# Kernel optimization log

Hardware: AMD Instinct MI355X
Metric: run time of the kernel (lower is better)

The kernel has to match this reference:

```python
import jax, jax.numpy as jnp
import numpy as np

PRE_NMS_TOPN = 12000
POST_NMS_TOPN = 2000
NMS_THRESH = 0.7
IM_SIZE = 1024
BATCH = 16
FPN_SCALES = np.array([8.0, 16.0, 32.0, 64.0, 128.0])
FPN_STRIDES = np.array([4, 8, 16, 32, 64])
RATIOS = np.array([0.5, 1.0, 2.0])
FEAT_SHAPES = [(IM_SIZE // s, IM_SIZE // s) for s in FPN_STRIDES]


def _anchors_single(scale, ratios, shape, stride):
    # faithful to generate_anchors_single_pyramid (mask-rcnn/FPN style)
    heights = scale / np.sqrt(ratios)
    widths = scale * np.sqrt(ratios)
    shifts_y = np.arange(0, shape[0]) * stride
    shifts_x = np.arange(0, shape[1]) * stride
    sx, sy = np.meshgrid(shifts_x, shifts_y)
    bw, bcx = np.meshgrid(widths, sx.flatten())
    bh, bcy = np.meshgrid(heights, sy.flatten())
    centers = np.stack([bcy, bcx], axis=2).reshape(-1, 2)
    sizes = np.stack([bh, bw], axis=2).reshape(-1, 2)
    return np.concatenate([centers - 0.5 * sizes, centers + 0.5 * sizes], axis=1)


def generate_anchors_all_pyramids():
    levels = [_anchors_single(FPN_SCALES[i], RATIOS, FEAT_SHAPES[i], FPN_STRIDES[i]) for i in range(5)]
    return np.concatenate(levels, axis=0).astype(np.float32)  # [261888, 4]


def setup_inputs() -> dict:
    key = jax.random.key(0)
    k1, k2 = jax.random.split(key)
    anchors = jnp.asarray(generate_anchors_all_pyramids())
    n = anchors.shape[0]
    scores = jax.random.uniform(k1, (BATCH, n), dtype=jnp.float32)
    bbox_deltas = jax.random.normal(k2, (BATCH, n, 4), dtype=jnp.float32) * 0.1
    im_info = jnp.tile(jnp.array([[IM_SIZE, IM_SIZE, 1.0]], dtype=jnp.float32), (BATCH, 1))
    return {"scores": scores, "bbox_deltas": bbox_deltas, "im_info": im_info, "anchors": anchors}


def _bbox_transform_inv(anchors, deltas):
    # anchors [N,4], deltas [B,N,4] -> [B,N,4]
    w = anchors[:, 2] - anchors[:, 0] + 1.0
    h = anchors[:, 3] - anchors[:, 1] + 1.0
    cx = anchors[:, 0] + 0.5 * w
    cy = anchors[:, 1] + 0.5 * h
    dx, dy, dw, dh = deltas[..., 0], deltas[..., 1], deltas[..., 2], deltas[..., 3]
    pcx = dx * w + cx
    pcy = dy * h + cy
    pw = jnp.exp(dw) * w
    ph = jnp.exp(dh) * h
    return jnp.stack([pcx - 0.5 * pw, pcy - 0.5 * ph, pcx + 0.5 * pw, pcy + 0.5 * ph], axis=-1)


def _clip_boxes(boxes, im_info):
    xmax = (im_info[:, 1] - 1.0)[:, None]
    ymax = (im_info[:, 0] - 1.0)[:, None]
    x1 = jnp.clip(boxes[..., 0], 0.0, xmax)
    y1 = jnp.clip(boxes[..., 1], 0.0, ymax)
    x2 = jnp.clip(boxes[..., 2], 0.0, xmax)
    y2 = jnp.clip(boxes[..., 3], 0.0, ymax)
    return jnp.stack([x1, y1, x2, y2], axis=-1)


def _nms_single(boxes):
    # boxes [P,4] sorted by score desc; greedy IoU suppression, keep POST_NMS_TOPN
    x1, y1, x2, y2 = boxes[:, 0], boxes[:, 1], boxes[:, 2], boxes[:, 3]
    areas = (x2 - x1 + 1.0) * (y2 - y1 + 1.0)

    def step(valid, _):
        any_valid = jnp.any(valid)
        idx = jnp.argmax(valid)  # first surviving box (sorted order)
        xx1 = jnp.maximum(x1[idx], x1)
        yy1 = jnp.maximum(y1[idx], y1)
        xx2 = jnp.minimum(x2[idx], x2)
        yy2 = jnp.minimum(y2[idx], y2)
        inter = jnp.maximum(xx2 - xx1 + 1.0, 0.0) * jnp.maximum(yy2 - yy1 + 1.0, 0.0)
        iou = inter / (areas[idx] + areas - inter)
        valid = valid & (iou <= NMS_THRESH)  # suppresses idx itself (IoU=1)
        return valid, jnp.where(any_valid, idx, -1)

    valid0 = jnp.ones(boxes.shape[0], dtype=bool)
    _, keep = jax.lax.scan(step, valid0, None, length=POST_NMS_TOPN)
    return keep  # [POST_NMS_TOPN] int, -1 = padding


def reference(scores, bbox_deltas, im_info, anchors):
    b = scores.shape[0]
    proposals = _bbox_transform_inv(anchors, bbox_deltas)  # [B,N,4]
    proposals = _clip_boxes(proposals, im_info)
    _, order = jax.lax.top_k(scores, PRE_NMS_TOPN)  # descending sort + pre-NMS cut
    props = jnp.take_along_axis(proposals, order[..., None], axis=1)  # [B,P,4]
    keep = jax.vmap(_nms_single)(props)  # [B,POST_NMS_TOPN]
    mask = (keep >= 0)
    kept = jnp.take_along_axis(props, jnp.maximum(keep, 0)[..., None], axis=1)
    kept = kept * mask[..., None].astype(props.dtype)  # zero-pad like output.zero_()
    batch_col = jnp.broadcast_to(jnp.arange(b, dtype=props.dtype)[:, None, None], (b, POST_NMS_TOPN, 1))
    return jnp.concatenate([batch_col, kept], axis=-1)  # [B,2000,5]
```

## Files before the change

kernel.cpp:

```cpp
#include <hip/hip_runtime.h>
#include <stdint.h>
#include <math.h>

#define NANCH 261888
#define NBATCH 16
#define PRE_NMS 12000
#define POST_NMS 2000
#define NBINS 21845
#define BINCAP 98304
#define NCHUNK 188
#define VBINS 4096
#define CANDCAP 16384
#define ADJR 12
#define OVFCAP 4096

__device__ __forceinline__ uint64_t make_key(float s, int i) {
    uint32_t u = __float_as_uint(s);
    u ^= (u >> 31) ? 0xFFFFFFFFu : 0x80000000u;
    return ((uint64_t)u << 32) | (uint32_t)(~(uint32_t)i);
}

__device__ __forceinline__ bool kill_pair(float4 a, float4 c) {
    const double MD = (double)0.7f + 2.9802322387695312e-08;
    float xx1 = fmaxf(a.x, c.x), yy1 = fmaxf(a.y, c.y);
    float xx2 = fminf(a.z, c.z), yy2 = fminf(a.w, c.w);
    float ww = fmaxf(__fadd_rn(__fsub_rn(xx2, xx1), 1.0f), 0.0f);
    float hh = fmaxf(__fadd_rn(__fsub_rn(yy2, yy1), 1.0f), 0.0f);
    float inter = __fmul_rn(ww, hh);
    float aa = __fmul_rn(__fadd_rn(__fsub_rn(a.z, a.x), 1.0f),
                         __fadd_rn(__fsub_rn(a.w, a.y), 1.0f));
    float ab = __fmul_rn(__fadd_rn(__fsub_rn(c.z, c.x), 1.0f),
                         __fadd_rn(__fsub_rn(c.w, c.y), 1.0f));
    float denom = __fsub_rn(__fadd_rn(aa, ab), inter);
    return !((double)inter < MD * (double)denom);
}

__device__ __forceinline__ int vbucket(float s) {
    int bk = (int)(s * 4096.0f);
    return min(max(bk, 0), VBINS - 1);
}

__global__ void k_init(uint32_t* hist, uint32_t* cnt, uint32_t* ccnt,
                       uint32_t* ovfc, uint32_t* deg) {
    int tid = blockIdx.x * 256 + threadIdx.x;
    int stride = gridDim.x * 256;
    for (int i = tid; i < NBATCH * VBINS; i += stride) hist[i] = 0;
    for (int i = tid; i < NBATCH * PRE_NMS; i += stride) deg[i] = 0;
    if (tid < NBATCH) { cnt[tid] = 0; ccnt[tid] = 0; ovfc[tid] = 0; }
}

__global__ __launch_bounds__(256) void k_histv(const float* __restrict__ scores,
                                               uint32_t* __restrict__ hist) {
    __shared__ uint32_t lh[VBINS];
    int tid = threadIdx.x;
    int b = blockIdx.y;
    for (int i = tid; i < VBINS; i += 256) lh[i] = 0;
    __syncthreads();
    const float* sc = scores + (size_t)b * NANCH;
    for (int i = blockIdx.x * 256 + tid; i < NANCH; i += gridDim.x * 256)
        atomicAdd(&lh[vbucket(sc[i])], 1u);
    __syncthreads();
    for (int i = tid; i < VBINS; i += 256) {
        uint32_t c = lh[i];
        if (c) atomicAdd(&hist[b * VBINS + i], c);
    }
}

__global__ __launch_bounds__(64) void k_pickv(const uint32_t* __restrict__ hist,
                                              uint32_t* __restrict__ Bsel) {
    int b = blockIdx.x;
    int ln = threadIdx.x;
    const uint32_t* h = hist + b * VBINS;
    int hi = VBINS - 1 - 64 * ln;
    uint32_t tot = 0;
    for (int k = 0; k < 64; ++k) tot += h[hi - k];
    uint32_t x = tot;
    for (int d = 1; d < 64; d <<= 1) { uint32_t y = __shfl_up(x, d); if (ln >= d) x += y; }
    uint32_t excl = x - tot;
    bool hitc = (excl < (uint32_t)PRE_NMS) && (excl + tot >= (uint32_t)PRE_NMS);
    unsigned long long bal = __ballot(hitc);
    int L = __ffsll(bal) - 1;
    if (ln == L) {
        uint32_t cum = excl;
        for (int k = 0; k < 64; ++k) {
            int bin = hi - k;
            uint32_t c = h[bin];
            if (cum + c >= (uint32_t)PRE_NMS) { Bsel[b] = (uint32_t)bin; break; }
            cum += c;
        }
    }
}

__global__ __launch_bounds__(256) void k_splitv(const float* __restrict__ scores,
                                                const uint32_t* __restrict__ Bsel,
                                                uint32_t* __restrict__ cnt,
                                                uint32_t* __restrict__ ccnt,
                                                uint64_t* __restrict__ selk,
                                                uint64_t* __restrict__ candbuf) {
    __shared__ uint64_t lbuf[2048];
    __shared__ uint32_t lcnt, lccnt, lbase, lcbase;
    int tid = threadIdx.x;
    int b = blockIdx.y;
    int ln = tid & 63;
    if (tid == 0) { lcnt = 0; lccnt = 0; }
    __syncthreads();
    uint32_t B = Bsel[b];
    const float* sc = scores + (size_t)b * NANCH;
    int base0 = blockIdx.x * 2048;
    for (int r = 0; r < 8; ++r) {
        int i = base0 + r * 256 + tid;
        bool psel = false, pcand = false;
        uint64_t key = 0;
        if (i < NANCH) {
            float s = sc[i];
            int bk = vbucket(s);
            psel = ((uint32_t)bk > B);
            pcand = ((uint32_t)bk == B);
            if (psel || pcand) key = make_key(s, i);
        }
        unsigned long long bs = __ballot(psel);
        uint32_t wb = 0;
        if (ln == 0 && bs) wb = atomicAdd(&lcnt, (uint32_t)__popcll(bs));
        wb = __shfl(wb, 0);
        if (psel) lbuf[wb + (uint32_t)__popcll(bs & ((1ull << ln) - 1ull))] = key;
        unsigned long long bcm = __ballot(pcand);
        uint32_t wc = 0;
        if (ln == 0 && bcm) wc = atomicAdd(&lccnt, (uint32_t)__popcll(bcm));
        wc = __shfl(wc, 0);
        if (pcand) lbuf[2047 - (wc + (uint32_t)__popcll(bcm & ((1ull << ln) - 1ull)))] = key;
    }
    __syncthreads();
    if (tid == 0) {
        lbase = lcnt ? atomicAdd(&cnt[b], lcnt) : 0u;
        lcbase = lccnt ? atomicAdd(&ccnt[b], lccnt) : 0u;
    }
    __syncthreads();
    uint32_t n = lcnt, bsx = lbase;
    for (uint32_t i = tid; i < n; i += 256)
        selk[(size_t)b * PRE_NMS + bsx + i] = lbuf[i];
    uint32_t nc = lccnt, bcx = lcbase;
    for (uint32_t i = tid; i < nc; i += 256) {
        uint32_t p = bcx + i;
        if (p < CANDCAP) candbuf[(size_t)b * CANDCAP + p] = lbuf[2047 - i];
    }
}

__global__ __launch_bounds__(1024) void k_rankb(const uint64_t* __restrict__ selk,
                                                const uint64_t* __restrict__ candbuf,
                                                const uint32_t* __restrict__ cnt,
                                                const uint32_t* __restrict__ ccnt,
                                                uint32_t* __restrict__ aidx) {
    __shared__ uint64_t kys[PRE_NMS];
    __shared__ uint32_t bbase[2048];
    __shared__ uint32_t bcur[2048];
    __shared__ uint16_t blist[PRE_NMS];
    __shared__ float redf[32];
    __shared__ uint32_t wsum[16];
    __shared__ uint32_t appcnt;
    int b = blockIdx.x, t = threadIdx.x, wv = t >> 6, ln = t & 63;
    const uint64_t* sk = selk + (size_t)b * PRE_NMS;
    const uint64_t* cb = candbuf + (size_t)b * CANDCAP;
    int nc = (int)cnt[b];
    int m = (int)min(ccnt[b], (uint32_t)CANDCAP);
    uint32_t nd = (uint32_t)(PRE_NMS - nc);
    if (t == 0) appcnt = 0;
    for (int i = t; i < 2048; i += 1024) bcur[i] = 0;
    float lmin = 1e30f, lmax = -1e30f;
    for (int i = t; i < nc; i += 1024) {
        uint64_t k = sk[i];
        kys[i] = k;
        float s = __uint_as_float((uint32_t)(k >> 32) ^ 0x80000000u);
        lmin = fminf(lmin, s); lmax = fmaxf(lmax, s);
    }
    __syncthreads();
    for (int i = t; i < m; i += 1024) {
        uint64_t ki = cb[i];
        int rk = 0;
        for (int j = 0; j < m; ++j) rk += (cb[j] > ki) ? 1 : 0;
        if ((uint32_t)rk < nd) {
            uint32_t pos = (uint32_t)nc + atomicAdd(&appcnt, 1u);
            kys[pos] = ki;
            float s = __uint_as_float((uint32_t)(ki >> 32) ^ 0x80000000u);
            lmin = fminf(lmin, s); lmax = fmaxf(lmax, s);
        }
    }
    for (int d = 1; d < 64; d <<= 1) {
        lmin = fminf(lmin, __shfl_xor(lmin, d));
        lmax = fmaxf(lmax, __shfl_xor(lmax, d));
    }
    if (ln == 0) { redf[wv] = lmin; redf[16 + wv] = lmax; }
    __syncthreads();
    float smin = redf[0], smax = redf[16];
    for (int w = 1; w < 16; ++w) { smin = fminf(smin, redf[w]); smax = fmaxf(smax, redf[16 + w]); }
    float scale = 2047.0f / fmaxf(smax - smin, 1e-20f);
    for (int i = t; i < PRE_NMS; i += 1024) {
        float s = __uint_as_float((uint32_t)(kys[i] >> 32) ^ 0x80000000u);
        int bk = min(max((int)((s - smin) * scale), 0), 2047);
        atomicAdd(&bcur[bk], 1u);
    }
    __syncthreads();
    {
        int r0 = 2 * t;
        uint32_t a0 = bcur[2047 - r0];
        uint32_t a1 = bcur[2046 - r0];
        uint32_t tot = a0 + a1;
        uint32_t x = tot;
        for (int d = 1; d < 64; d <<= 1) { uint32_t y = __shfl_up(x, d); if (ln >= d) x += y; }
        if (ln == 63) wsum[wv] = x;
        __syncthreads();
        uint32_t wb = 0;
        for (int w = 0; w < 16; ++w) wb += (w < wv) ? wsum[w] : 0u;
        uint32_t excl = wb + x - tot;
        bbase[2047 - r0] = excl;
        bbase[2046 - r0] = excl + a0;
        bcur[2047 - r0] = excl;
        bcur[2046 - r0] = excl + a0;
    }
    __syncthreads();
    for (int i = t; i < PRE_NMS; i += 1024) {
        float s = __uint_as_float((uint32_t)(kys[i] >> 32) ^ 0x80000000u);
        int bk = min(max((int)((s - smin) * scale), 0), 2047);
        uint32_t pos = atomicAdd(&bcur[bk], 1u);
        blist[pos] = (uint16_t)i;
    }
    __syncthreads();
    for (int i = t; i < PRE_NMS; i += 1024) {
        uint64_t ki = kys[i];
        float s = __uint_as_float((uint32_t)(ki >> 32) ^ 0x80000000u);
        int bk = min(max((int)((s - smin) * scale), 0), 2047);
        uint32_t start = bbase[bk], end = bcur[bk];
        int rk = 0;
        for (uint32_t p = start; p < end; ++p) {
            int j = (int)blist[p];
            rk += (kys[j] > ki) ? 1 : 0;
        }
        aidx[(size_t)b * PRE_NMS + bbase[bk] + (uint32_t)rk] = ~(uint32_t)(ki & 0xFFFFFFFFull);
    }
}

__global__ void k_gather(const float4* __restrict__ anchors, const float4* __restrict__ deltas,
                         const float* __restrict__ im_info, const uint32_t* __restrict__ aidx,
                         float4* __restrict__ props) {
    int b = blockIdx.y;
    int i = blockIdx.x * 256 + threadIdx.x;
    if (i >= PRE_NMS) return;
    uint32_t a = aidx[(size_t)b * PRE_NMS + i];
    float4 an = anchors[a];
    float4 dl = deltas[(size_t)b * NANCH + a];
    float w  = __fadd_rn(__fsub_rn(an.z, an.x), 1.0f);
    float h  = __fadd_rn(__fsub_rn(an.w, an.y), 1.0f);
    float cx = __fadd_rn(an.x, __fmul_rn(0.5f, w));
    float cy = __fadd_rn(an.y, __fmul_rn(0.5f, h));
    float pcx = __fadd_rn(__fmul_rn(dl.x, w), cx);
    float pcy = __fadd_rn(__fmul_rn(dl.y, h), cy);
    float ew = (float)exp((double)dl.z);
    float eh = (float)exp((double)dl.w);
    float pw = __fmul_rn(ew, w);
    float ph = __fmul_rn(eh, h);
    float x1 = __fsub_rn(pcx, __fmul_rn(0.5f, pw));
    float y1 = __fsub_rn(pcy, __fmul_rn(0.5f, ph));
    float x2 = __fadd_rn(pcx, __fmul_rn(0.5f, pw));
    float y2 = __fadd_rn(pcy, __fmul_rn(0.5f, ph));
    float xmax = __fsub_rn(im_info[b * 3 + 1], 1.0f);
    float ymax = __fsub_rn(im_info[b * 3 + 0], 1.0f);
    x1 = fminf(fmaxf(x1, 0.0f), xmax);
    y1 = fminf(fmaxf(y1, 0.0f), ymax);
    x2 = fminf(fmaxf(x2, 0.0f), xmax);
    y2 = fminf(fmaxf(y2, 0.0f), ymax);
    props[(size_t)b * PRE_NMS + i] = make_float4(x1, y1, x2, y2);
}

__device__ __forceinline__ int bucket_of(float w) {
    int iw = (int)w;
    int bb = 31 - __clz(iw);
    return min(max(bb, 2), 9);
}
__device__ __forceinline__ int grid_base(int g) {
    return (65536 - (65536 >> ((g - 2) * 2))) / 3;
}

__global__ __launch_bounds__(1024) void k_binfused(const float4* __restrict__ props,
                                                   uint32_t* __restrict__ binoff,
                                                   uint16_t* __restrict__ binlist) {
    __shared__ uint32_t bc[NBINS];
    __shared__ uint32_t wsum[16];
    int b = blockIdx.x, t = threadIdx.x, wv = t >> 6, ln = t & 63;
    for (int i = t; i < NBINS; i += 1024) bc[i] = 0;
    __syncthreads();
    const float4* pb = props + (size_t)b * PRE_NMS;
    for (int i = t; i < PRE_NMS; i += 1024) {
        float4 p = pb[i];
        float w = __fadd_rn(__fsub_rn(p.z, p.x), 1.0f);
        int bb = bucket_of(w);
        int cs = bb + 1, dim = 128 >> (bb - 2);
        int gb = grid_base(bb);
        int cx0 = ((int)p.x) >> cs, cx1 = ((int)p.z) >> cs;
        int cy0 = ((int)p.y) >> cs, cy1 = ((int)p.w) >> cs;
        for (int cy = cy0; cy <= cy1; ++cy)
            for (int cx = cx0; cx <= cx1; ++cx)
                atomicAdd(&bc[gb + cy * dim + cx], 1u);
    }
    __syncthreads();
    {
        const int PER = 22;
        int i0 = t * PER;
        uint32_t v[PER];
        uint32_t tot = 0;
        #pragma unroll
        for (int k = 0; k < PER; ++k) { int i = i0 + k; v[k] = (i < NBINS) ? bc[i] : 0; tot += v[k]; }
        uint32_t x = tot;
        for (int d = 1; d < 64; d <<= 1) { uint32_t y = __shfl_up(x, d); if (ln >= d) x += y; }
        if (ln == 63) wsum[wv] = x;
        __syncthreads();
        uint32_t wb = 0;
        for (int w = 0; w < 16; ++w) wb += (w < wv) ? wsum[w] : 0u;
        uint32_t run = wb + x - tot;
        uint32_t* offb = binoff + (size_t)b * (NBINS + 1);
        #pragma unroll
        for (int k = 0; k < PER; ++k) {
            int i = i0 + k;
            if (i < NBINS) { offb[i] = run; bc[i] = run; run += v[k]; }
        }
        if (t == 1023) offb[NBINS] = run;
    }
    __syncthreads();
    uint16_t* bl = binlist + (size_t)b * BINCAP;
    for (int i = t; i < PRE_NMS; i += 1024) {
        float4 p = pb[i];
        float w = __fadd_rn(__fsub_rn(p.z, p.x), 1.0f);
        int bb = bucket_of(w);
        int cs = bb + 1, dim = 128 >> (bb - 2);
        int gb = grid_base(bb);
        int cx0 = ((int)p.x) >> cs, cx1 = ((int)p.z) >> cs;
        int cy0 = ((int)p.y) >> cs, cy1 = ((int)p.w) >> cs;
        for (int cy = cy0; cy <= cy1; ++cy)
            for (int cx = cx0; cx <= cx1; ++cx) {
                uint32_t pos = atomicAdd(&bc[gb + cy * dim + cx], 1u);
                uint32_t e = (uint32_t)i | ((cx == cx0) ? 0x4000u : 0u)
                                        | ((cy == cy0) ? 0x8000u : 0u);
                if (pos < BINCAP) bl[pos] = (uint16_t)e;
            }
    }
}

__global__ __launch_bounds__(256) void k_search(const float4* __restrict__ props,
                                                const uint32_t* __restrict__ binoff,
                                                const uint16_t* __restrict__ binlist,
                                                uint32_t* __restrict__ deg,
                                                uint16_t* __restrict__ adjfix,
                                                uint32_t* __restrict__ ovf,
                                                uint32_t* __restrict__ ovfcnt) {
    int L = blockIdx.x;
    int b = L & (NBATCH - 1);
    int t = threadIdx.x;
    int i = (L >> 4) * 128 + (t >> 1);
    int half = t & 1;
    if (i >= PRE_NMS) return;
    const float4* pb = props + (size_t)b * PRE_NMS;
    float4 pi = pb[i];
    float wi = __fadd_rn(__fsub_rn(pi.z, pi.x), 1.0f);
    float hi = __fadd_rn(__fsub_rn(pi.w, pi.y), 1.0f);
    int bb = bucket_of(wi);
    const uint32_t* ob = binoff + (size_t)b * (NBINS + 1);
    const uint16_t* bl = binlist + (size_t)b * BINCAP;
    uint32_t* degb = deg + (size_t)b * PRE_NMS;
    uint16_t* adjb = adjfix + (size_t)b * PRE_NMS * ADJR;
    uint32_t* ovfb = ovf + (size_t)b * OVFCAP;
    float ex0 = fmaxf(__fsub_rn(pi.x, 1.0f), 0.0f);
    float ey0 = fmaxf(__fsub_rn(pi.y, 1.0f), 0.0f);
    float ex1 = fminf(__fadd_rn(pi.z, 1.0f), 1023.0f);
    float ey1 = fminf(__fadd_rn(pi.w, 1.0f), 1023.0f);

    auto add_edge = [&](int r, int n) {
        uint32_t s = atomicAdd(&degb[r], 1u);
        if (s < ADJR) {
            adjb[(size_t)r * ADJR + s] = (uint16_t)n;
        } else {
            uint32_t p = atomicAdd(&ovfcnt[b], 1u);
            if (p < OVFCAP) ovfb[p] = ((uint32_t)r << 16) | (uint32_t)n;
        }
    };

    #pragma unroll
    for (int pass = 0; pass < 2; ++pass) {
        int g = (pass == 0) ? bb : bb - 1;
        bool tie = (pass == 0);
        if (g < 2) continue;
        int cs = g + 1, dim = 128 >> (g - 2);
        int gb2 = grid_base(g);
        int sx0 = ((int)ex0) >> cs, sx1 = ((int)ex1) >> cs;
        int sy0 = ((int)ey0) >> cs, sy1 = ((int)ey1) >> cs;
        for (int cy = sy0; cy <= sy1; ++cy)
            for (int cx = sx0; cx <= sx1; ++cx) {
                int bin = gb2 + cy * dim + cx;
                uint32_t k0 = ob[bin], k1 = ob[bin + 1];
                for (uint32_t k = k0 + (uint32_t)half; k < k1; k += 2) {
                    uint32_t ent = bl[k];
                    int j = (int)(ent & 0x3FFFu);
                    if (tie && j <= i) continue;
                    if (!((cx == sx0) || (ent & 0x4000u))) continue;
                    if (!((cy == sy0) || (ent & 0x8000u))) continue;
                    float4 pj = pb[j];
                    float wj = __fadd_rn(__fsub_rn(pj.z, pj.x), 1.0f);
                    float hj = __fadd_rn(__fsub_rn(pj.w, pj.y), 1.0f);
                    if (fminf(wi, wj) < 0.6f * fmaxf(wi, wj)) continue;
                    if (fminf(hi, hj) < 0.6f * fmaxf(hi, hj)) continue;
                    if (kill_pair(pi, pj)) {
                        add_edge(i, j);
                        add_edge(j, i);
                    }
                }
            }
    }
}

__global__ __launch_bounds__(64) void k_greedy(const uint32_t* __restrict__ deg,
                                               const uint16_t* __restrict__ adjfix,
                                               const uint32_t* __restrict__ ovf,
                                               const uint32_t* __restrict__ ovfcnt,
                                               const float4* __restrict__ props,
                                               float* __restrict__ out) {
    int b = blockIdx.x;
    int ln = threadIdx.x;
    __shared__ uint32_t mask[375];
    __shared__ int keeps[POST_NMS];
    for (int i = ln; i < 375; i += 64) mask[i] = 0xFFFFFFFFu;
    const uint32_t* degb = deg + (size_t)b * PRE_NMS;
    const uint32_t* roww = (const uint32_t*)(adjfix + (size_t)b * PRE_NMS * ADJR);
    const uint32_t* ovfb = ovf + (size_t)b * OVFCAP;
    int novf = (int)min(ovfcnt[b], (uint32_t)OVFCAP);
    int nsel = 0;
    uint32_t dcur = (ln < PRE_NMS) ? degb[ln] : 0u;
    uint32_t w[6];
    #pragma unroll
    for (int k = 0; k < 6; ++k) w[k] = (ln < PRE_NMS) ? roww[(size_t)ln * 6 + k] : 0u;
    for (int c = 0; c < NCHUNK && nsel < POST_NMS; ++c) {
        int rn = (c + 1) * 64 + ln;
        uint32_t dnxt = 0, wn[6] = {0, 0, 0, 0, 0, 0};
        if (rn < PRE_NMS) {
            dnxt = degb[rn];
            #pragma unroll
            for (int k = 0; k < 6; ++k) wn[k] = roww[(size_t)rn * 6 + k];
        }
        int r = c * 64 + ln;
        bool inb = (r < PRE_NMS);
        int nfix = inb ? min((int)dcur, ADJR) : 0;
        uint32_t base = (uint32_t)(c * 64);
        uint64_t K = 0;
        #pragma unroll
        for (int k = 0; k < ADJR; ++k) {
            if (k < nfix) {
                uint32_t e = (w[k >> 1] >> ((k & 1) * 16)) & 0xFFFFu;
                uint32_t d = e - base;
                if (d < 64u) K |= (1ull << d);
            }
        }
        if (novf && inb) {
            for (int k = 0; k < novf; ++k) {
                uint32_t e = ovfb[k];
                if ((int)(e >> 16) == r) {
                    uint32_t d = (e & 0xFFFFu) - base;
                    if (d < 64u) K |= (1ull << d);
                }
            }
        }
        int vbit = inb ? (int)((mask[r >> 5] >> (r & 31)) & 1u) : 0;
        uint64_t valid = (uint64_t)__ballot(vbit);
        uint32_t Klo = (uint32_t)K, Khi = (uint32_t)(K >> 32);
        uint64_t todo = valid & (uint64_t)__ballot(K != 0);
        while (todo) {
            int s = __ffsll((unsigned long long)todo) - 1;
            if ((valid >> s) & 1ull) {
                uint32_t kl = (uint32_t)__builtin_amdgcn_readlane((int)Klo, s);
                uint32_t kh = (uint32_t)__builtin_amdgcn_readlane((int)Khi, s);
                valid &= ~(((uint64_t)kh << 32) | (uint64_t)kl);
            }
            todo &= (todo - 1);
            todo &= valid;
        }
        uint64_t acc = valid;
        int cnt2 = __popcll(acc);
        int myacc = (int)((acc >> ln) & 1ull);
        uint64_t ltm = (ln == 0) ? 0ull : (~0ull >> (64 - ln));
        int pos = nsel + __popcll(acc & ltm);
        bool eff = myacc && (pos < POST_NMS);
        if (eff) {
            keeps[pos] = r;
            #pragma unroll
            for (int k = 0; k < ADJR; ++k) {
                if (k < nfix) {
                    uint32_t e = (w[k >> 1] >> ((k & 1) * 16)) & 0xFFFFu;
                    atomicAnd(&mask[e >> 5], ~(1u << (e & 31)));
                }
            }
            if (novf) {
                for (int k = 0; k < novf; ++k) {
                    uint32_t e = ovfb[k];
                    if ((int)(e >> 16) == r) {
                        uint32_t n2 = e & 0xFFFFu;
                        atomicAnd(&mask[n2 >> 5], ~(1u << (n2 & 31)));
                    }
                }
            }
        }
        nsel += cnt2;
        dcur = dnxt;
        #pragma unroll
        for (int k = 0; k < 6; ++k) w[k] = wn[k];
    }
    __syncthreads();
    int n = min(nsel, POST_NMS);
    const float4* pb = props + (size_t)b * PRE_NMS;
    float* outb = out + (size_t)b * POST_NMS * 5;
    for (int r = ln; r < POST_NMS; r += 64) {
        float* row = outb + (size_t)r * 5;
        if (r < n) {
            float4 p = pb[keeps[r]];
            row[0] = (float)b; row[1] = p.x; row[2] = p.y; row[3] = p.z; row[4] = p.w;
        } else {
            row[0] = (float)b; row[1] = 0.0f; row[2] = 0.0f; row[3] = 0.0f; row[4] = 0.0f;
        }
    }
}

extern "C" void kernel_launch(void* const* d_in, const int* in_sizes, int n_in,
                              void* d_out, int out_size, void* d_ws, size_t ws_size,
                              hipStream_t stream) {
    const float* scores  = (const float*)d_in[0];
    const float* deltas  = (const float*)d_in[1];
    const float* im_info = (const float*)d_in[2];
    const float* anchors = (const float*)d_in[3];
    float* out = (float*)d_out;

    uint8_t* w = (uint8_t*)d_ws;
    uint32_t* hist    = (uint32_t*)(w);
    uint32_t* cnt     = (uint32_t*)(w + 262144);
    uint32_t* ccnt    = (uint32_t*)(w + 262208);
    uint32_t* Bsel    = (uint32_t*)(w + 262272);
    uint32_t* ovfcnt  = (uint32_t*)(w + 262400);
    uint64_t* selk    = (uint64_t*)(w + 262464);
    uint64_t* candbuf = (uint64_t*)(w + 1798464);
    uint32_t* aidx    = (uint32_t*)(w + 3895616);
    float*    props   = (float*)(w + 4663616);
    uint32_t* binoff  = (uint32_t*)(w + 7735616);
    uint16_t* binlist = (uint16_t*)(w + 9133760);
    uint32_t* deg     = (uint32_t*)(w + 12279488);
    uint16_t* adjfix  = (uint16_t*)(w + 13047488);
    uint32_t* ovf     = (uint32_t*)(w + 17655488);

    hipLaunchKernelGGL(k_init, dim3(256), dim3(256), 0, stream, hist, cnt, ccnt, ovfcnt, deg);
    hipLaunchKernelGGL(k_histv, dim3(32, NBATCH), dim3(256), 0, stream, scores, hist);
    hipLaunchKernelGGL(k_pickv, dim3(NBATCH), dim3(64), 0, stream, hist, Bsel);
    hipLaunchKernelGGL(k_splitv, dim3(128, NBATCH), dim3(256), 0, stream,
                       scores, Bsel, cnt, ccnt, selk, candbuf);
    hipLaunchKernelGGL(k_rankb, dim3(NBATCH), dim3(1024), 0, stream,
                       selk, candbuf, cnt, ccnt, aidx);
    hipLaunchKernelGGL(k_gather, dim3(47, NBATCH), dim3(256), 0, stream,
                       (const float4*)anchors, (const float4*)deltas, im_info, aidx,
                       (float4*)props);
    hipLaunchKernelGGL(k_binfused, dim3(NBATCH), dim3(1024), 0, stream,
                       (const float4*)props, binoff, binlist);
    hipLaunchKernelGGL(k_search, dim3(94 * NBATCH), dim3(256), 0, stream,
                       (const float4*)props, binoff, binlist, deg, adjfix, ovf, ovfcnt);
    hipLaunchKernelGGL(k_greedy, dim3(NBATCH), dim3(64), 0, stream,
                       deg, adjfix, ovf, ovfcnt, (const float4*)props, out);
}
```

Baseline: 216.4 us.

## Split spatial binning kernel across grid levels with atomic segment allocation

The binning kernel previously ran one 1024-thread block per batch and processed all 21845 bins of every grid level. It now launches 8 blocks per batch, one per grid level. Each block scans only its own level's bins and reserves a contiguous segment of the bin list with an atomic on a per-batch cursor. Because segments no longer sit in level order, bin end offsets come from a new 16-bit per-bin count array that the search kernel reads. This adds parallelism to a kernel that used only 16 blocks, at the cost of each block rereading every proposal and filtering by level, plus an extra count load in the search kernel.

```diff
diff --git a/kernel.cpp b/kernel.cpp
--- a/kernel.cpp
+++ b/kernel.cpp
@@ -41,12 +41,12 @@
 }
 
 __global__ void k_init(uint32_t* hist, uint32_t* cnt, uint32_t* ccnt,
-                       uint32_t* ovfc, uint32_t* deg) {
+                       uint32_t* ovfc, uint32_t* deg, uint32_t* segcur) {
     int tid = blockIdx.x * 256 + threadIdx.x;
     int stride = gridDim.x * 256;
     for (int i = tid; i < NBATCH * VBINS; i += stride) hist[i] = 0;
     for (int i = tid; i < NBATCH * PRE_NMS; i += stride) deg[i] = 0;
-    if (tid < NBATCH) { cnt[tid] = 0; ccnt[tid] = 0; ovfc[tid] = 0; }
+    if (tid < NBATCH) { cnt[tid] = 0; ccnt[tid] = 0; ovfc[tid] = 0; segcur[tid] = 0; }
 }
 
 __global__ __launch_bounds__(256) void k_histv(const float* __restrict__ scores,
@@ -279,63 +279,71 @@
     return (65536 - (65536 >> ((g - 2) * 2))) / 3;
 }
 
-__global__ __launch_bounds__(1024) void k_binfused(const float4* __restrict__ props,
+__global__ __launch_bounds__(1024) void k_binfuse8(const float4* __restrict__ props,
                                                    uint32_t* __restrict__ binoff,
-                                                   uint16_t* __restrict__ binlist) {
-    __shared__ uint32_t bc[NBINS];
+                                                   uint16_t* __restrict__ bincnt16,
+                                                   uint16_t* __restrict__ binlist,
+                                                   uint32_t* __restrict__ segcur) {
+    __shared__ uint32_t bc[16384];
     __shared__ uint32_t wsum[16];
-    int b = blockIdx.x, t = threadIdx.x, wv = t >> 6, ln = t & 63;
-    for (int i = t; i < NBINS; i += 1024) bc[i] = 0;
+    __shared__ uint32_t stot, sbase;
+    int b = blockIdx.x;
+    int g = 2 + blockIdx.y;
+    int t = threadIdx.x, wv = t >> 6, ln = t & 63;
+    int cs = g + 1, dim = 128 >> (g - 2);
+    int dim2 = dim * dim;
+    int gb = grid_base(g);
+    for (int i = t; i < dim2; i += 1024) bc[i] = 0;
     __syncthreads();
     const float4* pb = props + (size_t)b * PRE_NMS;
     for (int i = t; i < PRE_NMS; i += 1024) {
         float4 p = pb[i];
         float w = __fadd_rn(__fsub_rn(p.z, p.x), 1.0f);
-        int bb = bucket_of(w);
-        int cs = bb + 1, dim = 128 >> (bb - 2);
-        int gb = grid_base(bb);
+        if (bucket_of(w) != g) continue;
         int cx0 = ((int)p.x) >> cs, cx1 = ((int)p.z) >> cs;
         int cy0 = ((int)p.y) >> cs, cy1 = ((int)p.w) >> cs;
         for (int cy = cy0; cy <= cy1; ++cy)
             for (int cx = cx0; cx <= cx1; ++cx)
-                atomicAdd(&bc[gb + cy * dim + cx], 1u);
-    }
-    __syncthreads();
-    {
-        const int PER = 22;
-        int i0 = t * PER;
-        uint32_t v[PER];
-        uint32_t tot = 0;
-        #pragma unroll
-        for (int k = 0; k < PER; ++k) { int i = i0 + k; v[k] = (i < NBINS) ? bc[i] : 0; tot += v[k]; }
-        uint32_t x = tot;
-        for (int d = 1; d < 64; d <<= 1) { uint32_t y = __shfl_up(x, d); if (ln >= d) x += y; }
-        if (ln == 63) wsum[wv] = x;
-        __syncthreads();
-        uint32_t wb = 0;
-        for (int w = 0; w < 16; ++w) wb += (w < wv) ? wsum[w] : 0u;
-        uint32_t run = wb + x - tot;
-        uint32_t* offb = binoff + (size_t)b * (NBINS + 1);
-        #pragma unroll
-        for (int k = 0; k < PER; ++k) {
-            int i = i0 + k;
-            if (i < NBINS) { offb[i] = run; bc[i] = run; run += v[k]; }
-        }
-        if (t == 1023) offb[NBINS] = run;
+                atomicAdd(&bc[cy * dim + cx], 1u);
+    }
+    __syncthreads();
+    int per = (dim2 + 1023) >> 10;
+    int i0 = t * per, i1 = min(i0 + per, dim2);
+    uint32_t tot = 0;
+    for (int k = i0; k < i1; ++k) tot += bc[k];
+    uint32_t x = tot;
+    for (int d = 1; d < 64; d <<= 1) { uint32_t y = __shfl_up(x, d); if (ln >= d) x += y; }
+    if (ln == 63) wsum[wv] = x;
+    __syncthreads();
+    uint32_t wb = 0;
+    for (int w2 = 0; w2 < 16; ++w2) wb += (w2 < wv) ? wsum[w2] : 0u;
+    uint32_t excl = wb + x - tot;
+    if (t == 1023) stot = excl + tot;
+    __syncthreads();
+    if (t == 0) sbase = atomicAdd(&segcur[b], stot);
+    __syncthreads();
+    uint32_t base = sbase;
+    uint32_t* offb = binoff + (size_t)b * (NBINS + 1);
+    uint16_t* cntb = bincnt16 + (size_t)b * NBINS;
+    uint32_t run = base + excl;
+    for (int k = i0; k < i1; ++k) {
+        uint32_t c = bc[k];
+        offb[gb + k] = run;
+        cntb[gb + k] = (uint16_t)c;
+        bc[k] = run;
+        run += c;
     }
     __syncthreads();
     uint16_t* bl = binlist + (size_t)b * BINCAP;
     for (int i = t; i < PRE_NMS; i += 1024) {
         float4 p = pb[i];
         float w = __fadd_rn(__fsub_rn(p.z, p.x), 1.0f);
-        int bb = bucket_of(w);
-        int cs = bb + 1, dim = 128 >> (bb - 2);
-        int gb = grid_base(bb);
+        if (bucket_of(w) != g) continue;
         int cx0 = ((int)p.x) >> cs, cx1 = ((int)p.z) >> cs;
         int cy0 = ((int)p.y) >> cs, cy1 = ((int)p.w) >> cs;
         for (int cy = cy0; cy <= cy1; ++cy)
             for (int cx = cx0; cx <= cx1; ++cx) {
-                uint32_t pos = atomicAdd(&bc[gb + cy * dim + cx], 1u);
+                uint32_t pos = atomicAdd(&bc[cy * dim + cx], 1u);
                 uint32_t e = (uint32_t)i | ((cx == cx0) ? 0x4000u : 0u)
                                         | ((cy == cy0) ? 0x8000u : 0u);
                 if (pos < BINCAP) bl[pos] = (uint16_t)e;
@@ -345,6 +353,7 @@
 
 __global__ __launch_bounds__(256) void k_search(const float4* __restrict__ props,
                                                 const uint32_t* __restrict__ binoff,
+                                                const uint16_t* __restrict__ bincnt16,
                                                 const uint16_t* __restrict__ binlist,
                                                 uint32_t* __restrict__ deg,
                                                 uint16_t* __restrict__ adjfix,
@@ -362,6 +371,7 @@
     float hi = __fadd_rn(__fsub_rn(pi.w, pi.y), 1.0f);
     int bb = bucket_of(wi);
     const uint32_t* ob = binoff + (size_t)b * (NBINS + 1);
+    const uint16_t* cb = bincnt16 + (size_t)b * NBINS;
     const uint16_t* bl = binlist + (size_t)b * BINCAP;
     uint32_t* degb = deg + (size_t)b * PRE_NMS;
     uint16_t* adjb = adjfix + (size_t)b * PRE_NMS * ADJR;
@@ -393,7 +403,8 @@
         for (int cy = sy0; cy <= sy1; ++cy)
             for (int cx = sx0; cx <= sx1; ++cx) {
                 int bin = gb2 + cy * dim + cx;
-                uint32_t k0 = ob[bin], k1 = ob[bin + 1];
+                uint32_t k0 = ob[bin];
+                uint32_t k1 = k0 + (uint32_t)cb[bin];
                 for (uint32_t k = k0 + (uint32_t)half; k < k1; k += 2) {
                     uint32_t ent = bl[k];
                     int j = (int)(ent & 0x3FFFu);
@@ -533,22 +544,25 @@
     float* out = (float*)d_out;
 
     uint8_t* w = (uint8_t*)d_ws;
-    uint32_t* hist    = (uint32_t*)(w);
-    uint32_t* cnt     = (uint32_t*)(w + 262144);
-    uint32_t* ccnt    = (uint32_t*)(w + 262208);
-    uint32_t* Bsel    = (uint32_t*)(w + 262272);
-    uint32_t* ovfcnt  = (uint32_t*)(w + 262400);
-    uint64_t* selk    = (uint64_t*)(w + 262464);
-    uint64_t* candbuf = (uint64_t*)(w + 1798464);
-    uint32_t* aidx    = (uint32_t*)(w + 3895616);
-    float*    props   = (float*)(w + 4663616);
-    uint32_t* binoff  = (uint32_t*)(w + 7735616);
-    uint16_t* binlist = (uint16_t*)(w + 9133760);
-    uint32_t* deg     = (uint32_t*)(w + 12279488);
-    uint16_t* adjfix  = (uint16_t*)(w + 13047488);
-    uint32_t* ovf     = (uint32_t*)(w + 17655488);
-
-    hipLaunchKernelGGL(k_init, dim3(256), dim3(256), 0, stream, hist, cnt, ccnt, ovfcnt, deg);
+    uint32_t* hist     = (uint32_t*)(w);
+    uint32_t* cnt      = (uint32_t*)(w + 262144);
+    uint32_t* ccnt     = (uint32_t*)(w + 262208);
+    uint32_t* Bsel     = (uint32_t*)(w + 262272);
+    uint32_t* segcur   = (uint32_t*)(w + 262336);
+    uint32_t* ovfcnt   = (uint32_t*)(w + 262400);
+    uint64_t* selk     = (uint64_t*)(w + 262464);
+    uint64_t* candbuf  = (uint64_t*)(w + 1798464);
+    uint32_t* aidx     = (uint32_t*)(w + 3895616);
+    float*    props    = (float*)(w + 4663616);
+    uint32_t* binoff   = (uint32_t*)(w + 7735616);
+    uint16_t* binlist  = (uint16_t*)(w + 9133760);
+    uint32_t* deg      = (uint32_t*)(w + 12279488);
+    uint16_t* adjfix   = (uint16_t*)(w + 13047488);
+    uint32_t* ovf      = (uint32_t*)(w + 17655488);
+    uint16_t* bincnt16 = (uint16_t*)(w + 17917632);
+
+    hipLaunchKernelGGL(k_init, dim3(256), dim3(256), 0, stream,
+                       hist, cnt, ccnt, ovfcnt, deg, segcur);
     hipLaunchKernelGGL(k_histv, dim3(32, NBATCH), dim3(256), 0, stream, scores, hist);
     hipLaunchKernelGGL(k_pickv, dim3(NBATCH), dim3(64), 0, stream, hist, Bsel);
     hipLaunchKernelGGL(k_splitv, dim3(128, NBATCH), dim3(256), 0, stream,
@@ -558,10 +572,11 @@
     hipLaunchKernelGGL(k_gather, dim3(47, NBATCH), dim3(256), 0, stream,
                        (const float4*)anchors, (const float4*)deltas, im_info, aidx,
                        (float4*)props);
-    hipLaunchKernelGGL(k_binfused, dim3(NBATCH), dim3(1024), 0, stream,
-                       (const float4*)props, binoff, binlist);
+    hipLaunchKernelGGL(k_binfuse8, dim3(NBATCH, 8), dim3(1024), 0, stream,
+                       (const float4*)props, binoff, bincnt16, binlist, segcur);
     hipLaunchKernelGGL(k_search, dim3(94 * NBATCH), dim3(256), 0, stream,
-                       (const float4*)props, binoff, binlist, deg, adjfix, ovf, ovfcnt);
+                       (const float4*)props, binoff, bincnt16, binlist,
+                       deg, adjfix, ovf, ovfcnt);
     hipLaunchKernelGGL(k_greedy, dim3(NBATCH), dim3(64), 0, stream,
                        deg, adjfix, ovf, ovfcnt, (const float4*)props, out);
 }
```

New measurement: 222.5 us. +2.8%, slower.
